# Kernel optimization log

Measured on AMD Instinct MI355X. Metric: run time of the kernel, lower is better.

## Reference

```python
import jax, jax.numpy as jnp
import numpy as np

RNN = 50
FEAT = 128
NCLS = 8
ALPHA = 0.3  # keras LeakyReLU default


def setup_inputs() -> dict:
    key = jax.random.key(0)
    ks = jax.random.split(key, 6)
    B, T = 256, 2048
    x = jax.random.normal(ks[0], (B, T, FEAT), dtype=jnp.float32)
    # GRU params (Keras layout: kernel [F,3H], recurrent [H,3H], bias [2,3H] for reset_after=True)
    W = jax.random.normal(ks[1], (FEAT, 3 * RNN), dtype=jnp.float32) / np.sqrt(FEAT)
    U = jax.random.normal(ks[2], (RNN, 3 * RNN), dtype=jnp.float32) / np.sqrt(RNN)
    b = jax.random.normal(ks[3], (2, 3 * RNN), dtype=jnp.float32) * 0.01
    W2 = jax.random.normal(ks[4], (RNN, NCLS), dtype=jnp.float32) / np.sqrt(RNN)
    b2 = jnp.zeros((NCLS,), dtype=jnp.float32)
    return {"inputs": x, "W": W, "U": U, "b": b, "W2": W2, "b2": b2}


def _gru_last_state(x, W, U, b):
    # x: [B,T,F] -> precompute input projections [T,B,3H]
    B = x.shape[0]
    xw = jnp.einsum("btf,fh->tbh", x, W) + b[0]
    h0 = jnp.zeros((B, RNN), dtype=x.dtype)

    def step(h, xt):
        inner = h @ U + b[1]                       # [B,3H]
        z = jax.nn.sigmoid(xt[:, :RNN] + inner[:, :RNN])
        r = jax.nn.sigmoid(xt[:, RNN:2 * RNN] + inner[:, RNN:2 * RNN])
        hh = jnp.tanh(xt[:, 2 * RNN:] + r * inner[:, 2 * RNN:])
        h_new = z * h + (1.0 - z) * hh
        return h_new, None

    h_last, _ = jax.lax.scan(step, h0, xw)
    return h_last  # [B,H]


def reference(inputs, W, U, b, W2, b2):
    h = _gru_last_state(inputs, W, U, b)
    h = jnp.where(h >= 0, h, ALPHA * h)            # LeakyReLU(0.3)
    logits = h @ W2 + b2
    return jax.nn.softmax(logits, axis=-1)
```

## Files before the change

### kernel.cpp

```cpp
#include <hip/hip_runtime.h>

typedef __attribute__((ext_vector_type(4))) float f32x4;
typedef _Float16 f16;
typedef __attribute__((ext_vector_type(2))) _Float16 f16x2;
typedef __attribute__((ext_vector_type(8))) _Float16 f16x8;

#define T_LEN 2048
#define B_SZ 256
#define FEATN 128
#define H 50
#define H3 150
#define XW_STRIDE 160

__device__ __forceinline__ float rcpf(float x) { return __builtin_amdgcn_rcpf(x); }

__device__ __forceinline__ float dot2f(f16x2 a, f16x2 b, float c) {
#if __has_builtin(__builtin_amdgcn_fdot2)
  return __builtin_amdgcn_fdot2(a, b, c, false);
#else
  return fmaf((float)a[1], (float)b[1], fmaf((float)a[0], (float)b[0], c));
#endif
}

__global__ __launch_bounds__(256) void xw_gemm(const float* __restrict__ x,
                                               const float* __restrict__ W,
                                               f16* __restrict__ xw) {
  __shared__ f16 Wt[160 * 136];
  const int tid = threadIdx.x;
  for (int idx = tid; idx < FEATN * H3; idx += 256) {
    int f = idx / H3;
    int n = idx - f * H3;
    Wt[n * 136 + f] = (f16)W[idx];
  }
  for (int idx = tid; idx < 10 * FEATN; idx += 256) {
    int n = H3 + (idx >> 7);
    int f = idx & 127;
    Wt[n * 136 + f] = (f16)0.f;
  }
  __syncthreads();

  const int wid = tid >> 6;
  const int lane = tid & 63;
  const int l15 = lane & 15;
  const int g = lane >> 4;
  const long row0 = (long)blockIdx.x * 128 + wid * 32;

  f16x8 a[2][4];
#pragma unroll
  for (int sub = 0; sub < 2; ++sub) {
    const float* xp = x + (row0 + sub * 16 + l15) * FEATN + g * 8;
#pragma unroll
    for (int kk = 0; kk < 4; ++kk) {
      f32x4 p0 = *(const f32x4*)(xp + kk * 32);
      f32x4 p1 = *(const f32x4*)(xp + kk * 32 + 4);
      f16x8 v;
      v[0] = (f16)p0[0]; v[1] = (f16)p0[1]; v[2] = (f16)p0[2]; v[3] = (f16)p0[3];
      v[4] = (f16)p1[0]; v[5] = (f16)p1[1]; v[6] = (f16)p1[2]; v[7] = (f16)p1[3];
      a[sub][kk] = v;
    }
  }

  for (int nt = 0; nt < 10; ++nt) {
    const f16* bp = &Wt[(nt * 16 + l15) * 136 + g * 8];
    f16x8 bf0 = *(const f16x8*)(bp);
    f16x8 bf1 = *(const f16x8*)(bp + 32);
    f16x8 bf2 = *(const f16x8*)(bp + 64);
    f16x8 bf3 = *(const f16x8*)(bp + 96);
    f32x4 acc0 = {0.f, 0.f, 0.f, 0.f};
    f32x4 acc1 = {0.f, 0.f, 0.f, 0.f};
    acc0 = __builtin_amdgcn_mfma_f32_16x16x32_f16(a[0][0], bf0, acc0, 0, 0, 0);
    acc0 = __builtin_amdgcn_mfma_f32_16x16x32_f16(a[0][1], bf1, acc0, 0, 0, 0);
    acc0 = __builtin_amdgcn_mfma_f32_16x16x32_f16(a[0][2], bf2, acc0, 0, 0, 0);
    acc0 = __builtin_amdgcn_mfma_f32_16x16x32_f16(a[0][3], bf3, acc0, 0, 0, 0);
    acc1 = __builtin_amdgcn_mfma_f32_16x16x32_f16(a[1][0], bf0, acc1, 0, 0, 0);
    acc1 = __builtin_amdgcn_mfma_f32_16x16x32_f16(a[1][1], bf1, acc1, 0, 0, 0);
    acc1 = __builtin_amdgcn_mfma_f32_16x16x32_f16(a[1][2], bf2, acc1, 0, 0, 0);
    acc1 = __builtin_amdgcn_mfma_f32_16x16x32_f16(a[1][3], bf3, acc1, 0, 0, 0);
    int col = nt * 16 + l15;
    if (col < H3) {
#pragma unroll
      for (int r = 0; r < 4; ++r) {
        long rowA = row0 + g * 4 + r;
        xw[rowA * XW_STRIDE + col] = (f16)acc0[r];
        xw[(rowA + 16) * XW_STRIDE + col] = (f16)acc1[r];
      }
    }
  }
}

__global__ __launch_bounds__(64, 1) void gru_head64(const f16* __restrict__ xw,
                                                    const float* __restrict__ U,
                                                    const float* __restrict__ bias,
                                                    const float* __restrict__ W2,
                                                    const float* __restrict__ b2,
                                                    float* __restrict__ out) {
  __shared__ __align__(4) f16 h_lds16[64];
  __shared__ float fin[52];
  __shared__ float red[8];
  const int l = threadIdx.x;
  const int b = blockIdx.x;
  const int lc = l < H ? l : H - 1;
  const bool act = l < H;
  const long base = (long)b * T_LEN * XW_STRIDE;

  f16x2 uz2[25], ur2[25], uh2[25];
#pragma unroll
  for (int c = 0; c < 25; ++c) {
    uz2[c][0] = (f16)U[(2 * c) * H3 + lc];
    uz2[c][1] = (f16)U[(2 * c + 1) * H3 + lc];
    ur2[c][0] = (f16)U[(2 * c) * H3 + H + lc];
    ur2[c][1] = (f16)U[(2 * c + 1) * H3 + H + lc];
    uh2[c][0] = (f16)U[(2 * c) * H3 + 2 * H + lc];
    uh2[c][1] = (f16)U[(2 * c + 1) * H3 + 2 * H + lc];
  }
  const float bz = bias[lc] + bias[H3 + lc];
  const float br = bias[H + lc] + bias[H3 + H + lc];
  const float b0h = bias[2 * H + lc];
  const float b1h = bias[H3 + 2 * H + lc];

  h_lds16[l] = (f16)0.f;

  float hreg = 0.f;

  f16 pz[8], pr[8], ph[8];
#pragma unroll
  for (int p = 0; p < 8; ++p) {
    long o = base + (long)p * XW_STRIDE;
    pz[p] = xw[o + lc];
    pr[p] = xw[o + H + lc];
    ph[p] = xw[o + 2 * H + lc];
  }

  const f16x2* hp2 = (const f16x2*)h_lds16;

  for (int t0 = 0; t0 < T_LEN; t0 += 8) {
#define STEP(P)                                                               \
    {                                                                         \
      float sz = bz, sr = br, sh = b1h;                                       \
      _Pragma("unroll")                                                       \
      for (int c = 0; c < 25; ++c) {                                          \
        f16x2 hv = hp2[c];                                                    \
        sz = dot2f(hv, uz2[c], sz);                                           \
        sr = dot2f(hv, ur2[c], sr);                                           \
        sh = dot2f(hv, uh2[c], sh);                                           \
      }                                                                       \
      float xzf = (float)pz[P];                                               \
      float xrf = (float)pr[P];                                               \
      float xhf = (float)ph[P];                                               \
      {                                                                       \
        int tn = (t0 + (P) + 8) & (T_LEN - 1);                                \
        long o = base + (long)tn * XW_STRIDE;                                 \
        pz[P] = xw[o + lc];                                                   \
        pr[P] = xw[o + H + lc];                                               \
        ph[P] = xw[o + 2 * H + lc];                                           \
      }                                                                       \
      float az = sz + xzf;                                                    \
      float ar = sr + xrf;                                                    \
      float zz = rcpf(1.f + __expf(-az));                                     \
      float rr = rcpf(1.f + __expf(-ar));                                     \
      float ah = fmaf(rr, sh, xhf + b0h);                                     \
      float th = fmaf(2.f, rcpf(1.f + __expf(-2.f * ah)), -1.f);              \
      hreg = fmaf(zz, hreg - th, th);                                         \
      h_lds16[l] = (f16)hreg;                                                 \
    }
    STEP(0) STEP(1) STEP(2) STEP(3) STEP(4) STEP(5) STEP(6) STEP(7)
#undef STEP
  }

  if (act) {
    fin[l] = hreg >= 0.f ? hreg : 0.3f * hreg;
  }
  if (l < 8) {
    float acc = b2[l];
#pragma unroll
    for (int j = 0; j < H; ++j) acc = fmaf(fin[j], W2[j * 8 + l], acc);
    red[l] = acc;
  }
  if (l < 8) {
    float m = red[0];
#pragma unroll
    for (int i = 1; i < 8; ++i) m = fmaxf(m, red[i]);
    float s = 0.f;
#pragma unroll
    for (int i = 0; i < 8; ++i) s += __expf(red[i] - m);
    out[b * 8 + l] = __expf(red[l] - m) / s;
  }
}

extern "C" void kernel_launch(void* const* d_in, const int* in_sizes, int n_in,
                              void* d_out, int out_size, void* d_ws, size_t ws_size,
                              hipStream_t stream) {
  const float* x = (const float*)d_in[0];
  const float* W = (const float*)d_in[1];
  const float* U = (const float*)d_in[2];
  const float* bias = (const float*)d_in[3];
  const float* W2 = (const float*)d_in[4];
  const float* b2 = (const float*)d_in[5];
  float* out = (float*)d_out;
  f16* xw = (f16*)d_ws;

  xw_gemm<<<4096, 256, 0, stream>>>(x, W, xw);
  gru_head64<<<256, 64, 0, stream>>>(xw, U, bias, W2, b2, out);
}
```

Baseline: 618.9 us.

## Batch 16 sequences per block and compute GRU recurrence with MFMA

```diff
diff --git a/kernel.cpp b/kernel.cpp
--- a/kernel.cpp
+++ b/kernel.cpp
@@ -6,21 +6,19 @@
 typedef __attribute__((ext_vector_type(8))) _Float16 f16x8;
 
 #define T_LEN 2048
-#define B_SZ 256
 #define FEATN 128
 #define H 50
 #define H3 150
 #define XW_STRIDE 160
 
+#define RPB 16
+#define THR2 512
+#define HT_STRIDE 72
+#define CT_STRIDE 17
+#define STG_F16 (RPB * XW_STRIDE)
+#define NSTG 5
+
 __device__ __forceinline__ float rcpf(float x) { return __builtin_amdgcn_rcpf(x); }
-
-__device__ __forceinline__ float dot2f(f16x2 a, f16x2 b, float c) {
-#if __has_builtin(__builtin_amdgcn_fdot2)
-  return __builtin_amdgcn_fdot2(a, b, c, false);
-#else
-  return fmaf((float)a[1], (float)b[1], fmaf((float)a[0], (float)b[0], c));
-#endif
-}
 
 __global__ __launch_bounds__(256) void xw_gemm(const float* __restrict__ x,
                                                const float* __restrict__ W,
@@ -88,102 +86,178 @@
   }
 }
 
-__global__ __launch_bounds__(64, 1) void gru_head64(const f16* __restrict__ xw,
-                                                    const float* __restrict__ U,
-                                                    const float* __restrict__ bias,
-                                                    const float* __restrict__ W2,
-                                                    const float* __restrict__ b2,
-                                                    float* __restrict__ out) {
-  __shared__ __align__(4) f16 h_lds16[64];
-  __shared__ float fin[52];
-  __shared__ float red[8];
-  const int l = threadIdx.x;
-  const int b = blockIdx.x;
-  const int lc = l < H ? l : H - 1;
-  const bool act = l < H;
-  const long base = (long)b * T_LEN * XW_STRIDE;
-
-  f16x2 uz2[25], ur2[25], uh2[25];
-#pragma unroll
-  for (int c = 0; c < 25; ++c) {
-    uz2[c][0] = (f16)U[(2 * c) * H3 + lc];
-    uz2[c][1] = (f16)U[(2 * c + 1) * H3 + lc];
-    ur2[c][0] = (f16)U[(2 * c) * H3 + H + lc];
-    ur2[c][1] = (f16)U[(2 * c + 1) * H3 + H + lc];
-    uh2[c][0] = (f16)U[(2 * c) * H3 + 2 * H + lc];
-    uh2[c][1] = (f16)U[(2 * c + 1) * H3 + 2 * H + lc];
-  }
-  const float bz = bias[lc] + bias[H3 + lc];
-  const float br = bias[H + lc] + bias[H3 + H + lc];
-  const float b0h = bias[2 * H + lc];
-  const float b1h = bias[H3 + 2 * H + lc];
-
-  h_lds16[l] = (f16)0.f;
-
-  float hreg = 0.f;
-
-  f16 pz[8], pr[8], ph[8];
-#pragma unroll
-  for (int p = 0; p < 8; ++p) {
-    long o = base + (long)p * XW_STRIDE;
-    pz[p] = xw[o + lc];
-    pr[p] = xw[o + H + lc];
-    ph[p] = xw[o + 2 * H + lc];
-  }
-
-  const f16x2* hp2 = (const f16x2*)h_lds16;
-
-  for (int t0 = 0; t0 < T_LEN; t0 += 8) {
-#define STEP(P)                                                               \
-    {                                                                         \
-      float sz = bz, sr = br, sh = b1h;                                       \
-      _Pragma("unroll")                                                       \
-      for (int c = 0; c < 25; ++c) {                                          \
-        f16x2 hv = hp2[c];                                                    \
-        sz = dot2f(hv, uz2[c], sz);                                           \
-        sr = dot2f(hv, ur2[c], sr);                                           \
-        sh = dot2f(hv, uh2[c], sh);                                           \
-      }                                                                       \
-      float xzf = (float)pz[P];                                               \
-      float xrf = (float)pr[P];                                               \
-      float xhf = (float)ph[P];                                               \
-      {                                                                       \
-        int tn = (t0 + (P) + 8) & (T_LEN - 1);                                \
-        long o = base + (long)tn * XW_STRIDE;                                 \
-        pz[P] = xw[o + lc];                                                   \
-        pr[P] = xw[o + H + lc];                                               \
-        ph[P] = xw[o + 2 * H + lc];                                           \
-      }                                                                       \
-      float az = sz + xzf;                                                    \
-      float ar = sr + xrf;                                                    \
-      float zz = rcpf(1.f + __expf(-az));                                     \
-      float rr = rcpf(1.f + __expf(-ar));                                     \
-      float ah = fmaf(rr, sh, xhf + b0h);                                     \
-      float th = fmaf(2.f, rcpf(1.f + __expf(-2.f * ah)), -1.f);              \
-      hreg = fmaf(zz, hreg - th, th);                                         \
-      h_lds16[l] = (f16)hreg;                                                 \
-    }
-    STEP(0) STEP(1) STEP(2) STEP(3) STEP(4) STEP(5) STEP(6) STEP(7)
-#undef STEP
-  }
-
-  if (act) {
-    fin[l] = hreg >= 0.f ? hreg : 0.3f * hreg;
-  }
-  if (l < 8) {
-    float acc = b2[l];
-#pragma unroll
-    for (int j = 0; j < H; ++j) acc = fmaf(fin[j], W2[j * 8 + l], acc);
-    red[l] = acc;
-  }
-  if (l < 8) {
-    float m = red[0];
-#pragma unroll
-    for (int i = 1; i < 8; ++i) m = fmaxf(m, red[i]);
+__global__ __launch_bounds__(512, 1) void gru_mfma(const f16* __restrict__ xw,
+                                                   const float* __restrict__ U,
+                                                   const float* __restrict__ bias,
+                                                   const float* __restrict__ W2,
+                                                   const float* __restrict__ b2,
+                                                   float* __restrict__ out) {
+  __shared__ __align__(16) f16 hT[RPB * HT_STRIDE];
+  __shared__ __align__(16) float CT[160 * CT_STRIDE];
+  __shared__ __align__(16) f16 stage[NSTG * STG_F16];
+
+  const int tid = threadIdx.x;
+  const int blk = blockIdx.x;
+  const int lane = tid & 63;
+  const int wv = tid >> 6;
+
+  for (int i = tid; i < RPB * HT_STRIDE; i += THR2) hT[i] = (f16)0.f;
+
+  const int ntile = (wv < 2) ? 2 : 1;
+  const int tile0 = (wv < 2) ? (2 * wv) : (wv + 2);
+  const int bcol = lane & 15;
+  const int bk0 = (lane >> 4) * 8;
+  f16x8 bf[2][2];
+#pragma unroll
+  for (int i = 0; i < 2; ++i) {
+    int nt = tile0 + i;
+#pragma unroll
+    for (int kh = 0; kh < 2; ++kh) {
+      f16x8 v;
+#pragma unroll
+      for (int j = 0; j < 8; ++j) {
+        int k = kh * 32 + bk0 + j;
+        int col = nt * 16 + bcol;
+        float uv = (i < ntile && k < H && col < H3) ? U[k * H3 + col] : 0.f;
+        v[j] = (f16)uv;
+      }
+      bf[i][kh] = v;
+    }
+  }
+
+  const int gk = lane;
+  const bool gact = gk < H;
+  const int gkc = gact ? gk : 0;
+  const float bzc = bias[gkc] + bias[H3 + gkc];
+  const float brc = bias[H + gkc] + bias[H3 + H + gkc];
+  const float b0h = bias[2 * H + gkc];
+  const float b1h = bias[H3 + 2 * H + gkc];
+  const int r0 = wv, r1 = wv + 8;
+  float h0 = 0.f, h1 = 0.f;
+
+  const bool issuer = (wv < NSTG);
+  const char* srcp = nullptr;
+  if (issuer) {
+    int p = wv * 1024 + lane * 16;
+    int prow = p / 320;
+    int pcolb = p - prow * 320;
+    srcp = (const char*)xw + ((size_t)(blk * RPB + prow) * T_LEN) * 320 + pcolb;
+  }
+
+  __syncthreads();
+
+  if (issuer) {
+#pragma unroll
+    for (int i = 0; i < 4; ++i) {
+      __builtin_amdgcn_global_load_lds(srcp, stage + i * STG_F16 + wv * 512, 16, 0, 0);
+      srcp += 320;
+    }
+  }
+
+  const int arow = lane & 15;
+  const int ag = lane >> 4;
+  const f16* aptr = hT + arow * HT_STRIDE + ag * 8;
+
+  int rb = 0;
+  int wb = 4 * STG_F16;
+
+  for (int t = 0; t < T_LEN; ++t) {
+    if (issuer) {
+      __builtin_amdgcn_global_load_lds(srcp, stage + wb + wv * 512, 16, 0, 0);
+      if (t < T_LEN - 5) srcp += 320;
+    }
+
+    f16x8 a0 = *(const f16x8*)(aptr);
+    f16x8 a1 = *(const f16x8*)(aptr + 32);
+
+    {
+      f32x4 acc = {0.f, 0.f, 0.f, 0.f};
+      acc = __builtin_amdgcn_mfma_f32_16x16x32_f16(a0, bf[0][0], acc, 0, 0, 0);
+      acc = __builtin_amdgcn_mfma_f32_16x16x32_f16(a1, bf[0][1], acc, 0, 0, 0);
+      float* cp = CT + (tile0 * 16 + bcol) * CT_STRIDE + ag * 4;
+      cp[0] = acc[0]; cp[1] = acc[1]; cp[2] = acc[2]; cp[3] = acc[3];
+    }
+    if (ntile == 2) {
+      f32x4 acc = {0.f, 0.f, 0.f, 0.f};
+      acc = __builtin_amdgcn_mfma_f32_16x16x32_f16(a0, bf[1][0], acc, 0, 0, 0);
+      acc = __builtin_amdgcn_mfma_f32_16x16x32_f16(a1, bf[1][1], acc, 0, 0, 0);
+      float* cp = CT + ((tile0 + 1) * 16 + bcol) * CT_STRIDE + ag * 4;
+      cp[0] = acc[0]; cp[1] = acc[1]; cp[2] = acc[2]; cp[3] = acc[3];
+    }
+
+    __builtin_amdgcn_sched_barrier(0);
+    asm volatile("s_waitcnt lgkmcnt(0)");
+    if (issuer) asm volatile("s_waitcnt vmcnt(15)");
+    __builtin_amdgcn_sched_barrier(0);
+    __builtin_amdgcn_s_barrier();
+
+    if (gact) {
+      {
+        float iz = CT[gk * CT_STRIDE + r0];
+        float ir = CT[(gk + H) * CT_STRIDE + r0];
+        float ih = CT[(gk + 2 * H) * CT_STRIDE + r0];
+        float xz = (float)stage[rb + r0 * XW_STRIDE + gk];
+        float xr = (float)stage[rb + r0 * XW_STRIDE + H + gk];
+        float xh = (float)stage[rb + r0 * XW_STRIDE + 2 * H + gk];
+        float az = iz + bzc + xz;
+        float ar = ir + brc + xr;
+        float zz = rcpf(1.f + __expf(-az));
+        float rr = rcpf(1.f + __expf(-ar));
+        float ah = fmaf(rr, ih + b1h, xh + b0h);
+        float th = fmaf(2.f, rcpf(1.f + __expf(-2.f * ah)), -1.f);
+        h0 = fmaf(zz, h0 - th, th);
+        hT[r0 * HT_STRIDE + gk] = (f16)h0;
+      }
+      {
+        float iz = CT[gk * CT_STRIDE + r1];
+        float ir = CT[(gk + H) * CT_STRIDE + r1];
+        float ih = CT[(gk + 2 * H) * CT_STRIDE + r1];
+        float xz = (float)stage[rb + r1 * XW_STRIDE + gk];
+        float xr = (float)stage[rb + r1 * XW_STRIDE + H + gk];
+        float xh = (float)stage[rb + r1 * XW_STRIDE + 2 * H + gk];
+        float az = iz + bzc + xz;
+        float ar = ir + brc + xr;
+        float zz = rcpf(1.f + __expf(-az));
+        float rr = rcpf(1.f + __expf(-ar));
+        float ah = fmaf(rr, ih + b1h, xh + b0h);
+        float th = fmaf(2.f, rcpf(1.f + __expf(-2.f * ah)), -1.f);
+        h1 = fmaf(zz, h1 - th, th);
+        hT[r1 * HT_STRIDE + gk] = (f16)h1;
+      }
+    }
+
+    __builtin_amdgcn_sched_barrier(0);
+    asm volatile("s_waitcnt lgkmcnt(0)");
+    __builtin_amdgcn_sched_barrier(0);
+    __builtin_amdgcn_s_barrier();
+
+    rb += STG_F16; if (rb == NSTG * STG_F16) rb = 0;
+    wb += STG_F16; if (wb == NSTG * STG_F16) wb = 0;
+  }
+
+  __syncthreads();
+  if (gact) {
+    CT[r0 * 64 + gk] = h0 >= 0.f ? h0 : 0.3f * h0;
+    CT[r1 * 64 + gk] = h1 >= 0.f ? h1 : 0.3f * h1;
+  }
+  __syncthreads();
+  if (tid < 128) {
+    int row = tid >> 3, o = tid & 7;
+    float acc = b2[o];
+#pragma unroll
+    for (int j = 0; j < H; ++j) acc = fmaf(CT[row * 64 + j], W2[j * 8 + o], acc);
+    CT[1024 + row * 8 + o] = acc;
+  }
+  __syncthreads();
+  if (tid < 128) {
+    int row = tid >> 3, o = tid & 7;
+    float m = CT[1024 + row * 8];
+#pragma unroll
+    for (int i = 1; i < 8; ++i) m = fmaxf(m, CT[1024 + row * 8 + i]);
     float s = 0.f;
 #pragma unroll
-    for (int i = 0; i < 8; ++i) s += __expf(red[i] - m);
-    out[b * 8 + l] = __expf(red[l] - m) / s;
+    for (int i = 0; i < 8; ++i) s += __expf(CT[1024 + row * 8 + i] - m);
+    out[(blk * RPB + row) * 8 + o] = __expf(CT[1024 + row * 8 + o] - m) / s;
   }
 }
 
@@ -200,5 +274,5 @@
   f16* xw = (f16*)d_ws;
 
   xw_gemm<<<4096, 256, 0, stream>>>(x, W, xw);
-  gru_head64<<<256, 64, 0, stream>>>(xw, U, bias, W2, b2, out);
+  gru_mfma<<<16, 512, 0, stream>>>(xw, U, bias, W2, b2, out);
 }
```

Result: slower. 2.046 ms (+230.5%).
